# Kernel optimization log

Hardware: AMD Instinct MI355X
Metric: run time of the kernel (lower is better)

The kernel has to match this reference:

```python
import jax, jax.numpy as jnp
import numpy as np

B, N, C, H, WS, SS = 16, 4096, 512, 8, 8, 4
HD = C // H
SCALE = HD ** -0.5
NW = N // WS  # number of mask windows (= 512)
B_ = B * NW   # windows-times-batch after the view(-1, WS, C)


def _make_mask():
    # faithful replication of create_mask(), including the non-standard
    # window_partition (reshape->transpose->reshape) used by the repo
    img = np.zeros(N, dtype=np.float32)
    img[N - WS:N - SS] = 1.0
    img[N - SS:] = 2.0
    # window_partition on (1, N, 1) then .view(-1, WS):
    mw = img.reshape(N // WS, WS).T.reshape(N // WS, WS)  # (NW, WS)
    am = mw[:, None, :] - mw[:, :, None]                   # (NW, WS, WS)
    return jnp.asarray(np.where(am != 0.0, -100.0, 0.0).astype(np.float32))

ATTN_MASK = _make_mask()  # (NW, WS, WS)


def _layernorm(x, w, b, eps=1e-5):
    mu = jnp.mean(x, axis=-1, keepdims=True)
    var = jnp.mean((x - mu) ** 2, axis=-1, keepdims=True)
    return (x - mu) * jax.lax.rsqrt(var + eps) * w + b


def setup_inputs() -> dict:
    key = jax.random.key(0)
    ks = jax.random.split(key, 8)
    s = 0.02
    return {
        'x': jax.random.normal(ks[0], (B, N, C), jnp.float32),
        'norm1_w': jnp.ones((C,), jnp.float32),
        'norm1_b': jnp.zeros((C,), jnp.float32),
        'qkv_w': jax.random.normal(ks[1], (C, 3 * C), jnp.float32) * s,
        'qkv_b': jnp.zeros((3 * C,), jnp.float32),
        'proj_w': jax.random.normal(ks[2], (C, C), jnp.float32) * s,
        'proj_b': jnp.zeros((C,), jnp.float32),
        'norm2_w': jnp.ones((C,), jnp.float32),
        'norm2_b': jnp.zeros((C,), jnp.float32),
        'mlp_w1': jax.random.normal(ks[3], (C, 4 * C), jnp.float32) * s,
        'mlp_b1': jnp.zeros((4 * C,), jnp.float32),
        'mlp_w2': jax.random.normal(ks[4], (4 * C, C), jnp.float32) * s,
        'mlp_b2': jnp.zeros((C,), jnp.float32),
    }


def reference(x, norm1_w, norm1_b, qkv_w, qkv_b, proj_w, proj_b,
              norm2_w, norm2_b, mlp_w1, mlp_b1, mlp_w2, mlp_b2):
    shortcut = x
    h = _layernorm(x, norm1_w, norm1_b)
    h = jnp.roll(h, -SS, axis=1)  # shift_size > 0
    # repo's window_partition: (B,N,C) -> (B, N//WS, WS, C) -> perm -> (B*WS, N//WS, C)
    win = h.reshape(B, N // WS, WS, C).transpose(0, 2, 1, 3)
    # then .view(-1, WS, C): reinterpret flat buffer as (B_, WS, C)
    win = win.reshape(B_, WS, C)
    qkv = (win @ qkv_w + qkv_b).reshape(B_, WS, 3, H, HD).transpose(2, 0, 3, 1, 4)
    q, k, v = qkv[0], qkv[1], qkv[2]              # (B_, H, WS, HD)
    attn = jnp.einsum('bhqd,bhkd->bhqk', q, k) * SCALE
    attn = attn.reshape(B, NW, H, WS, WS) + ATTN_MASK[None, :, None]
    attn = jax.nn.softmax(attn.reshape(B_, H, WS, WS), axis=-1)
    out = jnp.einsum('bhqk,bhkd->bqhd', attn, v).reshape(B_, WS, C)
    out = out @ proj_w + proj_b
    # repo's window_reverse on the (B_, WS, C) buffer
    out = out.reshape(B, N // WS, WS, C).transpose(0, 2, 1, 3).reshape(B, N, C)
    out = jnp.roll(out, SS, axis=1)
    x = shortcut + out
    h2 = _layernorm(x, norm2_w, norm2_b)
    h2 = jax.nn.gelu(h2 @ mlp_w1 + mlp_b1, approximate=False)
    return x + (h2 @ mlp_w2 + mlp_b2)
```

## Files before the change

kernel.cpp:

```cpp
#include <hip/hip_runtime.h>
#include <hip/hip_bf16.h>
#include <cstdint>
#include <cstddef>

typedef __hip_bfloat16 BF16;
typedef __bf16 bf16x8 __attribute__((ext_vector_type(8)));
typedef float floatx4 __attribute__((ext_vector_type(4)));

static constexpr size_t OFF_WQKV  = 0;
static constexpr size_t OFF_WPROJ = OFF_WQKV  + (size_t)1536 * 512 * 2;
static constexpr size_t OFF_W1    = OFF_WPROJ + (size_t)512 * 512 * 2;
static constexpr size_t OFF_W2    = OFF_W1    + (size_t)2048 * 512 * 2;
static constexpr size_t OFF_H     = OFF_W2    + (size_t)512 * 2048 * 2;
static constexpr size_t OFF_QKV   = OFF_H     + (size_t)65536 * 512 * 2;
static constexpr size_t OFF_ATTN  = OFF_QKV   + (size_t)65536 * 1536 * 2;
static constexpr size_t OFF_M     = OFF_QKV;

__global__ __launch_bounds__(256) void wprep_kernel(
    const float* __restrict__ W, BF16* __restrict__ Wt, int K, int N) {
  __shared__ float t[64][65];
  const int n0 = blockIdx.x * 64, k0 = blockIdx.y * 64;
  const int tid = threadIdx.x;
#pragma unroll
  for (int it = 0; it < 16; ++it) {
    int idx = it * 256 + tid;
    int r = idx >> 6, c = idx & 63;
    t[r][c] = W[(size_t)(k0 + r) * N + (n0 + c)];
  }
  __syncthreads();
#pragma unroll
  for (int it = 0; it < 16; ++it) {
    int idx = it * 256 + tid;
    int r = idx >> 6, c = idx & 63;
    Wt[(size_t)(n0 + r) * K + (k0 + c)] = __float2bfloat16(t[c][r]);
  }
}

__global__ __launch_bounds__(256) void ln_kernel(
    const float* __restrict__ x, const float* __restrict__ w,
    const float* __restrict__ b, BF16* __restrict__ out) {
  const int lane = threadIdx.x & 63;
  const size_t row = (size_t)blockIdx.x * 4 + (threadIdx.x >> 6);
  const float* xr = x + row * 512 + lane * 8;
  float xv[8], wv[8], bv[8];
  *(float4*)&xv[0] = *(const float4*)xr;
  *(float4*)&xv[4] = *(const float4*)(xr + 4);
  *(float4*)&wv[0] = *(const float4*)(w + lane * 8);
  *(float4*)&wv[4] = *(const float4*)(w + lane * 8 + 4);
  *(float4*)&bv[0] = *(const float4*)(b + lane * 8);
  *(float4*)&bv[4] = *(const float4*)(b + lane * 8 + 4);
  float s = 0.0f, ss = 0.0f;
#pragma unroll
  for (int t = 0; t < 8; ++t) { s += xv[t]; ss += xv[t] * xv[t]; }
#pragma unroll
  for (int o = 32; o > 0; o >>= 1) { s += __shfl_xor(s, o); ss += __shfl_xor(ss, o); }
  const float mu = s * (1.0f / 512.0f);
  const float var = ss * (1.0f / 512.0f) - mu * mu;
  const float rs = rsqrtf(var + 1e-5f);
  BF16 ob[8];
#pragma unroll
  for (int t = 0; t < 8; ++t)
    ob[t] = __float2bfloat16((xv[t] - mu) * rs * wv[t] + bv[t]);
  *(uint4*)(out + row * 512 + lane * 8) = *(const uint4*)ob;
}

__device__ __forceinline__ void gload16(const BF16* g, const char* l) {
  __builtin_amdgcn_global_load_lds(
      (const __attribute__((address_space(1))) void*)g,
      (__attribute__((address_space(3))) void*)l, 16, 0, 0);
}

__device__ __forceinline__ int win_src_row(int r) {
  const int b = r >> 12;
  const int s = (r >> 9) & 7;
  const int mm = (r >> 3) & 63;
  const int j = r & 7;
  const int p = (64 * mm + 8 * j + s + 4) & 4095;
  return (b << 12) + p;
}

__device__ __forceinline__ float fast_gelu(float v) {
  const float t = __expf(v * -1.702f);
  return v * __builtin_amdgcn_rcpf(1.0f + t);
}

__device__ __forceinline__ uint2 pack4bf(float a, float b, float c, float d) {
  union { BF16 h[4]; uint2 u; } u;
  u.h[0] = __float2bfloat16(a); u.h[1] = __float2bfloat16(b);
  u.h[2] = __float2bfloat16(c); u.h[3] = __float2bfloat16(d);
  return u.u;
}

#define GATE4 asm volatile("s_waitcnt vmcnt(4)" ::: "memory")
#define GATE2 asm volatile("s_waitcnt vmcnt(2)" ::: "memory")
#define GATE0 asm volatile("s_waitcnt vmcnt(0)" ::: "memory")
#define GATEN asm volatile("" ::: "memory")
#define BAR() __builtin_amdgcn_s_barrier()
#define WAITL() asm volatile("s_waitcnt lgkmcnt(0)" ::: "memory")

template <int ROWMAP, int EPI, int K>
__global__ __launch_bounds__(512, 2) void gemm256(
    const BF16* __restrict__ A, const BF16* __restrict__ Bt,
    const float* __restrict__ bias, const float* __restrict__ resid,
    float* __restrict__ outf, BF16* __restrict__ outb, int Nout) {
  __shared__ __align__(16) char smem[131072];
  const int tid = threadIdx.x, lane = tid & 63, wv = tid >> 6;
  const int wm = wv >> 2, wn = wv & 3;

  const int gx = gridDim.x;
  const int nwg = gx * gridDim.y;
  const int hwid = blockIdx.y * gx + blockIdx.x;
  const int swz = (hwid & 7) * (nwg >> 3) + (hwid >> 3);
  const int bm = swz / gx, bn = swz - bm * gx;
  const int row0 = bm * 256, col0 = bn * 256;

  const int srow = lane >> 3;
  const int scol = ((lane & 7) ^ srow) * 8;
  const BF16* Pa[2][2];
  const BF16* Pb[2][2];
#pragma unroll
  for (int mh = 0; mh < 2; ++mh)
#pragma unroll
    for (int c = 0; c < 2; ++c) {
      int ra = row0 + mh * 128 + c * 64 + wv * 8 + srow;
      if (ROWMAP == 1) ra = win_src_row(ra);
      Pa[mh][c] = A + (size_t)ra * K + scol;
      const int rb = col0 + mh * 128 + c * 64 + wv * 8 + srow;
      Pb[mh][c] = Bt + (size_t)rb * K + scol;
    }
  const int ldsw = wv * 1024;

  const int r16 = lane & 15;
  const int sx0 = (((lane >> 4) + 0) ^ (r16 & 7)) * 16;
  const int sx1 = (((lane >> 4) + 4) ^ (r16 & 7)) * 16;
  const int raby = (wm * 64 + r16) * 128;
  const int rbby = (wn * 32 + r16) * 128;

  floatx4 acc[2][4][2][2];
#pragma unroll
  for (int mh = 0; mh < 2; ++mh)
#pragma unroll
    for (int m2 = 0; m2 < 4; ++m2)
#pragma unroll
      for (int nh = 0; nh < 2; ++nh)
#pragma unroll
        for (int n2 = 0; n2 < 2; ++n2)
          acc[mh][m2][nh][n2] = floatx4{0.f, 0.f, 0.f, 0.f};

  bf16x8 fa[4][2], fb0[2][2], fb1[2][2];

#define STG_A(half, dd) do {                                              \
    gload16(Pa[half][0], smem + (dd)*65536 + (half)*16384 + ldsw);        \
    gload16(Pa[half][1], smem + (dd)*65536 + (half)*16384 + 8192 + ldsw); \
  } while (0)
#define STG_B(half, dd) do {                                                      \
    gload16(Pb[half][0], smem + (dd)*65536 + 32768 + (half)*16384 + ldsw);        \
    gload16(Pb[half][1], smem + (dd)*65536 + 32768 + (half)*16384 + 8192 + ldsw); \
  } while (0)
#define ADV() do {                                          \
    Pa[0][0] += 64; Pa[0][1] += 64; Pa[1][0] += 64; Pa[1][1] += 64; \
    Pb[0][0] += 64; Pb[0][1] += 64; Pb[1][0] += 64; Pb[1][1] += 64; \
  } while (0)

#define RD_FA(mh, dd)                                                          \
  _Pragma("unroll")                                                            \
  for (int m2 = 0; m2 < 4; ++m2) {                                             \
    fa[m2][0] = *(const bf16x8*)(smem + (dd)*65536 + (mh)*16384 + raby + m2*2048 + sx0); \
    fa[m2][1] = *(const bf16x8*)(smem + (dd)*65536 + (mh)*16384 + raby + m2*2048 + sx1); \
  }
#define RD_FB(dst, nh, dd)                                                     \
  _Pragma("unroll")                                                            \
  for (int n2 = 0; n2 < 2; ++n2) {                                             \
    dst[n2][0] = *(const bf16x8*)(smem + (dd)*65536 + 32768 + (nh)*16384 + rbby + n2*2048 + sx0); \
    dst[n2][1] = *(const bf16x8*)(smem + (dd)*65536 + 32768 + (nh)*16384 + rbby + n2*2048 + sx1); \
  }
#define MF(mh, nh, fbx)                                                        \
  __builtin_amdgcn_s_setprio(1);                                               \
  _Pragma("unroll")                                                            \
  for (int ks = 0; ks < 2; ++ks)                                               \
    _Pragma("unroll")                                                          \
    for (int m2 = 0; m2 < 4; ++m2)                                             \
      _Pragma("unroll")                                                        \
      for (int n2 = 0; n2 < 2; ++n2)                                           \
        acc[mh][m2][nh][n2] = __builtin_amdgcn_mfma_f32_16x16x32_bf16(         \
            fbx[n2][ks], fa[m2][ks], acc[mh][m2][nh][n2], 0, 0, 0);            \
  __builtin_amdgcn_s_setprio(0)

  STG_A(0, 0);
  STG_B(0, 0);
  STG_B(1, 0);
  STG_A(1, 0);
  ADV();
  GATE4;
  BAR();

  constexpr int NT = K / 64;
  for (int t = 0; t < NT - 1; ++t) {
    const int dd = t & 1, de = dd ^ 1;
    RD_FA(0, dd); RD_FB(fb0, 0, dd);
    STG_A(0, de);
    BAR(); WAITL();
    MF(0, 0, fb0);
    GATE4; BAR();
    RD_FB(fb1, 1, dd);
    STG_B(0, de);
    BAR(); WAITL();
    MF(0, 1, fb1);
    GATE4; BAR();
    RD_FA(1, dd);
    STG_B(1, de);
    BAR(); WAITL();
    MF(1, 1, fb1);
    GATEN; BAR();
    STG_A(1, de);
    BAR(); WAITL();
    MF(1, 0, fb0);
    GATE4; BAR();
    ADV();
  }
  {
    const int dd = (NT - 1) & 1;
    RD_FA(0, dd); RD_FB(fb0, 0, dd);
    BAR(); WAITL();
    MF(0, 0, fb0);
    GATE2; BAR();
    RD_FB(fb1, 1, dd);
    BAR(); WAITL();
    MF(0, 1, fb1);
    GATE0; BAR();
    RD_FA(1, dd);
    BAR(); WAITL();
    MF(1, 1, fb1);
    GATEN; BAR();
    BAR(); WAITL();
    MF(1, 0, fb0);
  }
#undef STG_A
#undef STG_B
#undef ADV
#undef RD_FA
#undef RD_FB
#undef MF

  const int g4 = (lane >> 4) * 4;
  float4 bsv[2][2];
#pragma unroll
  for (int nh = 0; nh < 2; ++nh)
#pragma unroll
    for (int n2 = 0; n2 < 2; ++n2)
      bsv[nh][n2] = *(const float4*)&bias[col0 + nh * 128 + wn * 32 + n2 * 16 + g4];

#pragma unroll
  for (int mh = 0; mh < 2; ++mh)
#pragma unroll
    for (int m2 = 0; m2 < 4; ++m2) {
      const int r = row0 + mh * 128 + wm * 64 + m2 * 16 + r16;
      size_t rowbase;
      if (EPI == 2) {
        const int b = r >> 12;
        const int np = (r >> 3) & 511;
        const int ap = r & 7;
        const int io = ((ap << 9) + np + 4) & 4095;
        rowbase = ((size_t)(b << 12) + io) * 512;
      } else {
        rowbase = (size_t)r * Nout;
      }
#pragma unroll
      for (int nh = 0; nh < 2; ++nh)
#pragma unroll
        for (int n2 = 0; n2 < 2; ++n2) {
          const int c0 = col0 + nh * 128 + wn * 32 + n2 * 16 + g4;
          floatx4 v = acc[mh][m2][nh][n2];
          v[0] += bsv[nh][n2].x; v[1] += bsv[nh][n2].y;
          v[2] += bsv[nh][n2].z; v[3] += bsv[nh][n2].w;
          if (EPI == 0) {
            *(uint2*)&outb[rowbase + c0] = pack4bf(v[0], v[1], v[2], v[3]);
          } else if (EPI == 1) {
            *(uint2*)&outb[rowbase + c0] = pack4bf(
                fast_gelu(v[0]), fast_gelu(v[1]), fast_gelu(v[2]), fast_gelu(v[3]));
          } else if (EPI == 2) {
            const float4 rv = *(const float4*)&resid[rowbase + c0];
            float4 ov = {rv.x + v[0], rv.y + v[1], rv.z + v[2], rv.w + v[3]};
            *(float4*)&outf[rowbase + c0] = ov;
          } else {
            float4 ov = *(float4*)&outf[rowbase + c0];
            ov.x += v[0]; ov.y += v[1]; ov.z += v[2]; ov.w += v[3];
            *(float4*)&outf[rowbase + c0] = ov;
          }
        }
    }
}

__global__ __launch_bounds__(64) void attn_kernel(
    const BF16* __restrict__ qkv, BF16* __restrict__ out) {
  const int w = blockIdx.x;
  const int lane = threadIdx.x;
  const int qi = lane >> 3, kj = lane & 7;
  __shared__ __align__(16) BF16 sm[8 * 1544];
  const BF16* src = qkv + (size_t)w * 8 * 1536;
#pragma unroll
  for (int rr = 0; rr < 8; ++rr) {
    const uint4* s4 = (const uint4*)(src + (size_t)rr * 1536);
    uint4* d4 = (uint4*)(&sm[rr * 1544]);
#pragma unroll
    for (int c = 0; c < 3; ++c) d4[c * 64 + lane] = s4[c * 64 + lane];
  }
  __syncthreads();

  const int s = (w >> 6) & 7, mm = w & 63;
  const int pi = 64 * mm + 8 * qi + s;
  const int pj = 64 * mm + 8 * kj + s;
  const int ri = pi >= 4092 ? 2 : (pi >= 4088 ? 1 : 0);
  const int rj = pj >= 4092 ? 2 : (pj >= 4088 ? 1 : 0);
  const float maskv = (ri != rj) ? -100.0f : 0.0f;

  for (int h = 0; h < 8; ++h) {
    const BF16* qp = &sm[qi * 1544 + h * 64];
    const BF16* kp = &sm[kj * 1544 + 512 + h * 64];
    float acc = 0.0f;
#pragma unroll
    for (int d0 = 0; d0 < 8; ++d0) {
      bf16x8 qv = *(const bf16x8*)(qp + d0 * 8);
      bf16x8 kv = *(const bf16x8*)(kp + d0 * 8);
#pragma unroll
      for (int t = 0; t < 8; ++t) acc += (float)qv[t] * (float)kv[t];
    }
    float sc = acc * 0.125f + maskv;
    float mx = sc;
    mx = fmaxf(mx, __shfl_xor(mx, 1, 8));
    mx = fmaxf(mx, __shfl_xor(mx, 2, 8));
    mx = fmaxf(mx, __shfl_xor(mx, 4, 8));
    float e = __expf(sc - mx);
    float den = e;
    den += __shfl_xor(den, 1, 8);
    den += __shfl_xor(den, 2, 8);
    den += __shfl_xor(den, 4, 8);
    const float P = e / den;

    float o8[8];
#pragma unroll
    for (int t = 0; t < 8; ++t) o8[t] = 0.0f;
#pragma unroll
    for (int j2 = 0; j2 < 8; ++j2) {
      float p2 = __shfl(P, j2, 8);
      bf16x8 vv = *(const bf16x8*)(&sm[j2 * 1544 + 1024 + h * 64 + kj * 8]);
#pragma unroll
      for (int t = 0; t < 8; ++t) o8[t] += p2 * (float)vv[t];
    }
    BF16 ob[8];
#pragma unroll
    for (int t = 0; t < 8; ++t) ob[t] = __float2bfloat16(o8[t]);
    *(uint4*)(&out[((size_t)w * 8 + qi) * 512 + h * 64 + kj * 8]) = *(const uint4*)ob;
  }
}

extern "C" void kernel_launch(void* const* d_in, const int* in_sizes, int n_in,
                              void* d_out, int out_size, void* d_ws, size_t ws_size,
                              hipStream_t stream) {
  (void)in_sizes; (void)n_in; (void)out_size; (void)ws_size;
  const float* x     = (const float*)d_in[0];
  const float* n1w   = (const float*)d_in[1];
  const float* n1b   = (const float*)d_in[2];
  const float* qkvw  = (const float*)d_in[3];
  const float* qkvb  = (const float*)d_in[4];
  const float* projw = (const float*)d_in[5];
  const float* projb = (const float*)d_in[6];
  const float* n2w   = (const float*)d_in[7];
  const float* n2b   = (const float*)d_in[8];
  const float* w1    = (const float*)d_in[9];
  const float* b1    = (const float*)d_in[10];
  const float* w2    = (const float*)d_in[11];
  const float* b2    = (const float*)d_in[12];
  float* out = (float*)d_out;
  char* ws = (char*)d_ws;

  BF16* wt_qkv  = (BF16*)(ws + OFF_WQKV);
  BF16* wt_proj = (BF16*)(ws + OFF_WPROJ);
  BF16* wt_w1   = (BF16*)(ws + OFF_W1);
  BF16* wt_w2   = (BF16*)(ws + OFF_W2);
  BF16* hbuf    = (BF16*)(ws + OFF_H);
  BF16* qkvbuf  = (BF16*)(ws + OFF_QKV);
  BF16* attnbuf = (BF16*)(ws + OFF_ATTN);
  BF16* mbuf    = (BF16*)(ws + OFF_M);

  wprep_kernel<<<dim3(24, 8), 256, 0, stream>>>(qkvw, wt_qkv, 512, 1536);
  wprep_kernel<<<dim3(8, 8), 256, 0, stream>>>(projw, wt_proj, 512, 512);
  wprep_kernel<<<dim3(32, 8), 256, 0, stream>>>(w1, wt_w1, 512, 2048);
  wprep_kernel<<<dim3(8, 32), 256, 0, stream>>>(w2, wt_w2, 2048, 512);

  ln_kernel<<<16384, 256, 0, stream>>>(x, n1w, n1b, hbuf);
  gemm256<1, 0, 512><<<dim3(6, 256), 512, 0, stream>>>(hbuf, wt_qkv, qkvb, nullptr, nullptr, qkvbuf, 1536);
  attn_kernel<<<8192, 64, 0, stream>>>(qkvbuf, attnbuf);
  gemm256<0, 2, 512><<<dim3(2, 256), 512, 0, stream>>>(attnbuf, wt_proj, projb, x, out, nullptr, 512);
  ln_kernel<<<16384, 256, 0, stream>>>(out, n2w, n2b, hbuf);
  gemm256<0, 1, 512><<<dim3(8, 256), 512, 0, stream>>>(hbuf, wt_w1, b1, nullptr, nullptr, mbuf, 2048);
  gemm256<0, 3, 2048><<<dim3(2, 256), 512, 0, stream>>>(mbuf, wt_w2, b2, nullptr, out, nullptr, 512);
}
```

Before: 702.7 us.

## Make GEMM blocks persistent over multiple M tiles with cross-tile prefetch

Each GEMM workgroup now processes MT consecutive 256-row tiles, prefetching the next tile's A and B data during the last K step of the current tile so the pipeline does not drain between tiles. The epilogue is emitted per tile and the accumulators are reset afterwards. This is meant to cut pipeline fill and drain and per-block launch overhead. The cost is a smaller grid (e.g. 256 blocks for the MLP up-projection), which may leave CUs idle and cause tail imbalance.

New measurement: 1.045 ms. +48.8%, slower.

```diff
diff --git a/kernel.cpp b/kernel.cpp
--- a/kernel.cpp
+++ b/kernel.cpp
@@ -98,7 +98,7 @@
 #define BAR() __builtin_amdgcn_s_barrier()
 #define WAITL() asm volatile("s_waitcnt lgkmcnt(0)" ::: "memory")
 
-template <int ROWMAP, int EPI, int K>
+template <int ROWMAP, int EPI, int K, int MT>
 __global__ __launch_bounds__(512, 2) void gemm256(
     const BF16* __restrict__ A, const BF16* __restrict__ Bt,
     const float* __restrict__ bias, const float* __restrict__ resid,
@@ -112,7 +112,7 @@
   const int hwid = blockIdx.y * gx + blockIdx.x;
   const int swz = (hwid & 7) * (nwg >> 3) + (hwid >> 3);
   const int bm = swz / gx, bn = swz - bm * gx;
-  const int row0 = bm * 256, col0 = bn * 256;
+  const int row0 = bm * 256 * MT, col0 = bn * 256;
 
   const int srow = lane >> 3;
   const int scol = ((lane & 7) ^ srow) * 8;
@@ -135,6 +135,7 @@
   const int sx1 = (((lane >> 4) + 4) ^ (r16 & 7)) * 16;
   const int raby = (wm * 64 + r16) * 128;
   const int rbby = (wn * 32 + r16) * 128;
+  const int g4 = (lane >> 4) * 4;
 
   floatx4 acc[2][4][2][2];
 #pragma unroll
@@ -186,6 +187,63 @@
             fbx[n2][ks], fa[m2][ks], acc[mh][m2][nh][n2], 0, 0, 0);            \
   __builtin_amdgcn_s_setprio(0)
 
+#define EPILOG(rb0) do {                                                       \
+    float4 bsv[2][2];                                                          \
+    _Pragma("unroll")                                                          \
+    for (int nh = 0; nh < 2; ++nh)                                             \
+      _Pragma("unroll")                                                        \
+      for (int n2 = 0; n2 < 2; ++n2)                                           \
+        bsv[nh][n2] = *(const float4*)&bias[col0 + nh * 128 + wn * 32 + n2 * 16 + g4]; \
+    _Pragma("unroll")                                                          \
+    for (int mh = 0; mh < 2; ++mh)                                             \
+      _Pragma("unroll")                                                        \
+      for (int m2 = 0; m2 < 4; ++m2) {                                         \
+        const int r = (rb0) + mh * 128 + wm * 64 + m2 * 16 + r16;              \
+        size_t rowbase;                                                        \
+        if (EPI == 2) {                                                        \
+          const int b = r >> 12;                                               \
+          const int np = (r >> 3) & 511;                                       \
+          const int ap = r & 7;                                                \
+          const int io = ((ap << 9) + np + 4) & 4095;                          \
+          rowbase = ((size_t)(b << 12) + io) * 512;                            \
+        } else {                                                               \
+          rowbase = (size_t)r * Nout;                                          \
+        }                                                                      \
+        _Pragma("unroll")                                                      \
+        for (int nh = 0; nh < 2; ++nh)                                         \
+          _Pragma("unroll")                                                    \
+          for (int n2 = 0; n2 < 2; ++n2) {                                     \
+            const int c0 = col0 + nh * 128 + wn * 32 + n2 * 16 + g4;           \
+            floatx4 v = acc[mh][m2][nh][n2];                                   \
+            v[0] += bsv[nh][n2].x; v[1] += bsv[nh][n2].y;                      \
+            v[2] += bsv[nh][n2].z; v[3] += bsv[nh][n2].w;                      \
+            if (EPI == 0) {                                                    \
+              *(uint2*)&outb[rowbase + c0] = pack4bf(v[0], v[1], v[2], v[3]);  \
+            } else if (EPI == 1) {                                             \
+              *(uint2*)&outb[rowbase + c0] = pack4bf(                          \
+                  fast_gelu(v[0]), fast_gelu(v[1]), fast_gelu(v[2]), fast_gelu(v[3])); \
+            } else if (EPI == 2) {                                             \
+              const float4 rv = *(const float4*)&resid[rowbase + c0];          \
+              float4 ov = {rv.x + v[0], rv.y + v[1], rv.z + v[2], rv.w + v[3]};\
+              *(float4*)&outf[rowbase + c0] = ov;                              \
+            } else {                                                           \
+              float4 ov = *(float4*)&outf[rowbase + c0];                       \
+              ov.x += v[0]; ov.y += v[1]; ov.z += v[2]; ov.w += v[3];          \
+              *(float4*)&outf[rowbase + c0] = ov;                              \
+            }                                                                  \
+          }                                                                    \
+      }                                                                        \
+    _Pragma("unroll")                                                          \
+    for (int mh = 0; mh < 2; ++mh)                                             \
+      _Pragma("unroll")                                                        \
+      for (int m2 = 0; m2 < 4; ++m2)                                           \
+        _Pragma("unroll")                                                      \
+        for (int nh = 0; nh < 2; ++nh)                                         \
+          _Pragma("unroll")                                                    \
+          for (int n2 = 0; n2 < 2; ++n2)                                       \
+            acc[mh][m2][nh][n2] = floatx4{0.f, 0.f, 0.f, 0.f};                 \
+  } while (0)
+
   STG_A(0, 0);
   STG_B(0, 0);
   STG_B(1, 0);
@@ -195,45 +253,74 @@
   BAR();
 
   constexpr int NT = K / 64;
-  for (int t = 0; t < NT - 1; ++t) {
-    const int dd = t & 1, de = dd ^ 1;
-    RD_FA(0, dd); RD_FB(fb0, 0, dd);
-    STG_A(0, de);
-    BAR(); WAITL();
-    MF(0, 0, fb0);
-    GATE4; BAR();
-    RD_FB(fb1, 1, dd);
-    STG_B(0, de);
-    BAR(); WAITL();
-    MF(0, 1, fb1);
-    GATE4; BAR();
-    RD_FA(1, dd);
-    STG_B(1, de);
-    BAR(); WAITL();
-    MF(1, 1, fb1);
-    GATEN; BAR();
-    STG_A(1, de);
-    BAR(); WAITL();
-    MF(1, 0, fb0);
-    GATE4; BAR();
-    ADV();
-  }
-  {
-    const int dd = (NT - 1) & 1;
-    RD_FA(0, dd); RD_FB(fb0, 0, dd);
-    BAR(); WAITL();
-    MF(0, 0, fb0);
-    GATE2; BAR();
-    RD_FB(fb1, 1, dd);
-    BAR(); WAITL();
-    MF(0, 1, fb1);
-    GATE0; BAR();
-    RD_FA(1, dd);
-    BAR(); WAITL();
-    MF(1, 1, fb1);
-    GATEN; BAR();
-    BAR(); WAITL();
-    MF(1, 0, fb0);
+  int row0m = row0;
+
+  for (int mt = 0; mt < MT; ++mt) {
+    for (int t = 0; t < NT; ++t) {
+      const int dd = t & 1, de = dd ^ 1;
+      const bool last = (mt == MT - 1) && (t == NT - 1);
+      if (t == NT - 1 && !last) {
+        const int nbase = row0 + (mt + 1) * 256;
+        if (ROWMAP == 1) {
+#pragma unroll
+          for (int mh = 0; mh < 2; ++mh)
+#pragma unroll
+            for (int c = 0; c < 2; ++c) {
+              const int ra = win_src_row(nbase + mh * 128 + c * 64 + wv * 8 + srow);
+              Pa[mh][c] = A + (size_t)ra * K + scol;
+            }
+        } else {
+#pragma unroll
+          for (int mh = 0; mh < 2; ++mh)
+#pragma unroll
+            for (int c = 0; c < 2; ++c) Pa[mh][c] += (size_t)255 * K;
+        }
+#pragma unroll
+        for (int mh = 0; mh < 2; ++mh)
+#pragma unroll
+          for (int c = 0; c < 2; ++c) Pb[mh][c] -= K;
+      }
+
+      if (!last) {
+        RD_FA(0, dd); RD_FB(fb0, 0, dd);
+        STG_A(0, de);
+        BAR(); WAITL();
+        MF(0, 0, fb0);
+        GATE4; BAR();
+        RD_FB(fb1, 1, dd);
+        STG_B(0, de);
+        BAR(); WAITL();
+        MF(0, 1, fb1);
+        GATE4; BAR();
+        RD_FA(1, dd);
+        STG_B(1, de);
+        BAR(); WAITL();
+        MF(1, 1, fb1);
+        GATEN; BAR();
+        STG_A(1, de);
+        BAR(); WAITL();
+        MF(1, 0, fb0);
+        GATE4; BAR();
+        ADV();
+      } else {
+        RD_FA(0, dd); RD_FB(fb0, 0, dd);
+        BAR(); WAITL();
+        MF(0, 0, fb0);
+        GATE2; BAR();
+        RD_FB(fb1, 1, dd);
+        BAR(); WAITL();
+        MF(0, 1, fb1);
+        GATE0; BAR();
+        RD_FA(1, dd);
+        BAR(); WAITL();
+        MF(1, 1, fb1);
+        GATEN; BAR();
+        BAR(); WAITL();
+        MF(1, 0, fb0);
+      }
+    }
+    EPILOG(row0m);
+    row0m += 256;
   }
 #undef STG_A
 #undef STG_B
@@ -241,54 +328,7 @@
 #undef RD_FA
 #undef RD_FB
 #undef MF
-
-  const int g4 = (lane >> 4) * 4;
-  float4 bsv[2][2];
-#pragma unroll
-  for (int nh = 0; nh < 2; ++nh)
-#pragma unroll
-    for (int n2 = 0; n2 < 2; ++n2)
-      bsv[nh][n2] = *(const float4*)&bias[col0 + nh * 128 + wn * 32 + n2 * 16 + g4];
-
-#pragma unroll
-  for (int mh = 0; mh < 2; ++mh)
-#pragma unroll
-    for (int m2 = 0; m2 < 4; ++m2) {
-      const int r = row0 + mh * 128 + wm * 64 + m2 * 16 + r16;
-      size_t rowbase;
-      if (EPI == 2) {
-        const int b = r >> 12;
-        const int np = (r >> 3) & 511;
-        const int ap = r & 7;
-        const int io = ((ap << 9) + np + 4) & 4095;
-        rowbase = ((size_t)(b << 12) + io) * 512;
-      } else {
-        rowbase = (size_t)r * Nout;
-      }
-#pragma unroll
-      for (int nh = 0; nh < 2; ++nh)
-#pragma unroll
-        for (int n2 = 0; n2 < 2; ++n2) {
-          const int c0 = col0 + nh * 128 + wn * 32 + n2 * 16 + g4;
-          floatx4 v = acc[mh][m2][nh][n2];
-          v[0] += bsv[nh][n2].x; v[1] += bsv[nh][n2].y;
-          v[2] += bsv[nh][n2].z; v[3] += bsv[nh][n2].w;
-          if (EPI == 0) {
-            *(uint2*)&outb[rowbase + c0] = pack4bf(v[0], v[1], v[2], v[3]);
-          } else if (EPI == 1) {
-            *(uint2*)&outb[rowbase + c0] = pack4bf(
-                fast_gelu(v[0]), fast_gelu(v[1]), fast_gelu(v[2]), fast_gelu(v[3]));
-          } else if (EPI == 2) {
-            const float4 rv = *(const float4*)&resid[rowbase + c0];
-            float4 ov = {rv.x + v[0], rv.y + v[1], rv.z + v[2], rv.w + v[3]};
-            *(float4*)&outf[rowbase + c0] = ov;
-          } else {
-            float4 ov = *(float4*)&outf[rowbase + c0];
-            ov.x += v[0]; ov.y += v[1]; ov.z += v[2]; ov.w += v[3];
-            *(float4*)&outf[rowbase + c0] = ov;
-          }
-        }
-    }
+#undef EPILOG
 }
 
 __global__ __launch_bounds__(64) void attn_kernel(
@@ -389,10 +429,10 @@
   wprep_kernel<<<dim3(8, 32), 256, 0, stream>>>(w2, wt_w2, 2048, 512);
 
   ln_kernel<<<16384, 256, 0, stream>>>(x, n1w, n1b, hbuf);
-  gemm256<1, 0, 512><<<dim3(6, 256), 512, 0, stream>>>(hbuf, wt_qkv, qkvb, nullptr, nullptr, qkvbuf, 1536);
+  gemm256<1, 0, 512, 2><<<dim3(6, 128), 512, 0, stream>>>(hbuf, wt_qkv, qkvb, nullptr, nullptr, qkvbuf, 1536);
   attn_kernel<<<8192, 64, 0, stream>>>(qkvbuf, attnbuf);
-  gemm256<0, 2, 512><<<dim3(2, 256), 512, 0, stream>>>(attnbuf, wt_proj, projb, x, out, nullptr, 512);
+  gemm256<0, 2, 512, 2><<<dim3(2, 128), 512, 0, stream>>>(attnbuf, wt_proj, projb, x, out, nullptr, 512);
   ln_kernel<<<16384, 256, 0, stream>>>(out, n2w, n2b, hbuf);
-  gemm256<0, 1, 512><<<dim3(8, 256), 512, 0, stream>>>(hbuf, wt_w1, b1, nullptr, nullptr, mbuf, 2048);
-  gemm256<0, 3, 2048><<<dim3(2, 256), 512, 0, stream>>>(mbuf, wt_w2, b2, nullptr, out, nullptr, 512);
-}
+  gemm256<0, 1, 512, 8><<<dim3(8, 32), 512, 0, stream>>>(hbuf, wt_w1, b1, nullptr, nullptr, mbuf, 2048);
+  gemm256<0, 3, 2048, 2><<<dim3(2, 128), 512, 0, stream>>>(mbuf, wt_w2, b2, nullptr, out, nullptr, 512);
+}
```
